# Kernel optimization log

Hardware: AMD Instinct MI355X
Metric: run time of the kernel (lower is better)

Reference implementation:

```python
import jax, jax.numpy as jnp
import numpy as np

B, S, E, H = 2, 2048, 1024, 16
DH = E // H


def setup_inputs() -> dict:
    key = jax.random.key(0)
    ks = jax.random.split(key, 9)
    inp = {
        "query": jax.random.normal(ks[0], (B, S, E), dtype=jnp.float32),
        "key": jax.random.normal(ks[1], (B, S, E), dtype=jnp.float32),
        "value": jax.random.normal(ks[2], (B, S, E), dtype=jnp.float32),
        # causal mask: True means "masked out" (masked_fill semantics)
        "mask": jnp.broadcast_to(
            jnp.triu(jnp.ones((S, S), dtype=bool), k=1)[None, None], (B, 1, S, S)
        ),
        # learned parameters (nn.Linear weight is [out, in]; y = x @ W.T + b)
        "Wq": jax.random.normal(ks[3], (E, E), dtype=jnp.float32) / np.sqrt(E),
        "Wk": jax.random.normal(ks[4], (E, E), dtype=jnp.float32) / np.sqrt(E),
        "Wv": jax.random.normal(ks[5], (E, E), dtype=jnp.float32) / np.sqrt(E),
        "Wo": jax.random.normal(ks[6], (E, E), dtype=jnp.float32) / np.sqrt(E),
        "bo": jax.random.normal(ks[7], (E,), dtype=jnp.float32) * 0.01,
    }
    return inp


def reference(query, key, value, mask, Wq, Wk, Wv, Wo, bo):
    # projections (no bias for q/k/v)
    Q = query @ Wq.T  # [B,S,E]
    K = key @ Wk.T
    V = value @ Wv.T
    # split heads: [B,S,E] -> [B,H,S,Dh]
    Q = Q.reshape(B, S, H, DH).transpose(0, 2, 1, 3)
    K = K.reshape(B, S, H, DH).transpose(0, 2, 1, 3)
    V = V.reshape(B, S, H, DH).transpose(0, 2, 1, 3)
    scale = 1.0 / np.sqrt(DH).astype(np.float32)
    scores = jnp.einsum("bhqd,bhkd->bhqk", Q, K) * scale  # [B,H,S,S]
    scores = jnp.where(mask, -jnp.inf, scores)
    attn = jax.nn.softmax(scores, axis=-1)
    # dropout(p=0.2) is identity in eval mode
    out = jnp.einsum("bhqk,bhkd->bhqd", attn, V)  # [B,H,S,Dh]
    out = out.transpose(0, 2, 1, 3).reshape(B, S, E)
    return out @ Wo.T + bo
```

## Files before the change

### kernel.cpp

```cpp
#include <hip/hip_runtime.h>
#include <hip/hip_bf16.h>
#include <stdint.h>

#define Bb 2
#define Ss 2048
#define Ee 1024
#define Hh 16
#define Dh 64

typedef __bf16 bf16_t;
typedef __attribute__((ext_vector_type(8))) __bf16 bf16x8;
typedef __attribute__((ext_vector_type(4))) __bf16 bf16x4;
typedef __attribute__((ext_vector_type(4))) float f32x4;

#define QSCALE_LOG2E 0.18033688011112042f

__device__ inline void gload_lds16(const void* g, void* l) {
  __builtin_amdgcn_global_load_lds((__attribute__((address_space(1))) void*)g,
                                   (__attribute__((address_space(3))) void*)l,
                                   16, 0, 0);
}

__device__ inline void wg_barrier() {
  asm volatile("s_barrier" ::: "memory");
}

__device__ __forceinline__ int p_addr64(int q, int kv) {
  return q * 128 + ((((kv >> 3) ^ q) & 7) << 4) + (kv & 7) * 2;
}

struct Cvt7 {
  const float* s[7];
  bf16_t* d[7];
  int n8[7];
};

__global__ __launch_bounds__(256) void cvt_f32_bf16(Cvt7 c) {
  int gid = blockIdx.x * 256 + threadIdx.x;
#pragma unroll
  for (int j = 0; j < 7; ++j) {
    if (gid < c.n8[j]) {
      const float* s = c.s[j] + (size_t)gid * 8;
      const f32x4 lo = *(const f32x4*)s;
      const f32x4 hi = *(const f32x4*)(s + 4);
      bf16x8 v;
      v[0] = (bf16_t)lo[0]; v[1] = (bf16_t)lo[1];
      v[2] = (bf16_t)lo[2]; v[3] = (bf16_t)lo[3];
      v[4] = (bf16_t)hi[0]; v[5] = (bf16_t)hi[1];
      v[6] = (bf16_t)hi[2]; v[7] = (bf16_t)hi[3];
      *(bf16x8*)(c.d[j] + (size_t)gid * 8) = v;
      return;
    }
    gid -= c.n8[j];
  }
}

template <int ROWS>
__device__ __forceinline__ void stage_bf16(const bf16_t* __restrict__ src,
                                           int ldk, int k0, bf16_t* lds,
                                           int wave, int lane) {
  const int srow = lane >> 3, sslot = lane & 7;
#pragma unroll
  for (int r = 0; r < ROWS / 32; ++r) {
    const int chunk = wave + r * 4;
    const int row = chunk * 8 + srow;
    const int k16 = sslot ^ (row & 7);
    gload_lds16(src + (size_t)row * ldk + k0 + k16 * 8, lds + chunk * 512);
  }
}

template <typename EPI>
__device__ __forceinline__ void gemm_128x64(const bf16_t* Arow,
                                            const bf16_t* Wrow, bf16_t* As,
                                            bf16_t* Bs, int wave, int lane,
                                            EPI epi) {
  const int lr = lane & 15, lg = lane >> 4;
  f32x4 acc[2][4] = {};

  stage_bf16<128>(Arow, Ee, 0, As, wave, lane);
  stage_bf16<64>(Wrow, Ee, 0, Bs, wave, lane);
  stage_bf16<128>(Arow, Ee, 64, As + 8192, wave, lane);
  stage_bf16<64>(Wrow, Ee, 64, Bs + 4096, wave, lane);

  for (int t = 0; t < 16; ++t) {
    const int cur = t & 1;
    if (t < 15)
      asm volatile("s_waitcnt vmcnt(6)" ::: "memory");
    else
      asm volatile("s_waitcnt vmcnt(0)" ::: "memory");
    wg_barrier();

    const char* a_base = (const char*)(As + cur * 8192);
    const char* b_base = (const char*)(Bs + cur * 4096);
#pragma unroll
    for (int kk = 0; kk < 2; ++kk) {
      bf16x8 af[2], bfr[4];
#pragma unroll
      for (int x = 0; x < 2; ++x) {
        const int arow = wave * 32 + x * 16 + lr;
        af[x] = *(const bf16x8*)(a_base + ((arow * 128 + kk * 64 + lg * 16) ^
                                           ((arow & 7) << 4)));
      }
#pragma unroll
      for (int ni = 0; ni < 4; ++ni) {
        const int brow = ni * 16 + lr;
        bfr[ni] = *(const bf16x8*)(b_base + ((brow * 128 + kk * 64 + lg * 16) ^
                                             ((brow & 7) << 4)));
      }
#pragma unroll
      for (int mi = 0; mi < 2; ++mi)
#pragma unroll
        for (int ni = 0; ni < 4; ++ni)
          acc[mi][ni] = __builtin_amdgcn_mfma_f32_16x16x32_bf16(
              af[mi], bfr[ni], acc[mi][ni], 0, 0, 0);
    }
    wg_barrier();
    if (t + 2 < 16) {
      stage_bf16<128>(Arow, Ee, (t + 2) * 64, As + cur * 8192, wave, lane);
      stage_bf16<64>(Wrow, Ee, (t + 2) * 64, Bs + cur * 4096, wave, lane);
    }
  }

#pragma unroll
  for (int mi = 0; mi < 2; ++mi)
#pragma unroll
    for (int i = 0; i < 4; ++i) {
      const int mloc = wave * 32 + mi * 16 + lg * 4 + i;
#pragma unroll
      for (int ni = 0; ni < 4; ++ni)
        epi(mloc, ni * 16 + lr, acc[mi][ni][i]);
    }
}

__global__ __launch_bounds__(256) void qkv_proj(
    const bf16_t* __restrict__ Aq, const bf16_t* __restrict__ Ak,
    const bf16_t* __restrict__ Av, const bf16_t* __restrict__ Wq,
    const bf16_t* __restrict__ Wk, const bf16_t* __restrict__ Wv,
    bf16_t* __restrict__ Cq, bf16_t* __restrict__ Ck,
    bf16_t* __restrict__ Cv) {
  __shared__ bf16_t As[2][128 * 64];
  __shared__ bf16_t Bs[2][64 * 64];
  const int z = blockIdx.z;
  const bf16_t* A = (z == 0) ? Aq : (z == 1) ? Ak : Av;
  const bf16_t* W = (z == 0) ? Wq : (z == 1) ? Wk : Wv;
  bf16_t* C = (z == 0) ? Cq : (z == 1) ? Ck : Cv;

  const int wg = blockIdx.y * 16 + blockIdx.x;
  const int virt = (wg & 7) * 64 + (wg >> 3);
  const int n0 = (virt & 15) * 64, m0 = (virt >> 4) * 128;

  const int lane = threadIdx.x & 63, wave = threadIdx.x >> 6;

  gemm_128x64(A + (size_t)m0 * Ee, W + (size_t)n0 * Ee, As[0], Bs[0], wave,
              lane, [&](int mloc, int nloc, float v) {
                const int m = m0 + mloc, n = n0 + nloc;
                if (z == 0) v *= QSCALE_LOG2E;
                const int b = m >> 11, s = m & (Ss - 1);
                const int h = n >> 6, d = n & 63;
                if (z != 2)
                  C[(((size_t)(b * Hh + h)) * Ss + s) * Dh + d] = (bf16_t)v;
                else
                  C[(((size_t)(b * Hh + h)) * Dh + d) * Ss + s] = (bf16_t)v;
              });
}

__global__ __launch_bounds__(256) void out_gemm(const bf16_t* __restrict__ A,
                                                const bf16_t* __restrict__ W,
                                                const float* __restrict__ bias,
                                                float* __restrict__ C) {
  __shared__ bf16_t As[2][128 * 64];
  __shared__ bf16_t Bs[2][64 * 64];
  const int wg = blockIdx.y * 16 + blockIdx.x;
  const int virt = (wg & 7) * 64 + (wg >> 3);
  const int n0 = (virt & 15) * 64, m0 = (virt >> 4) * 128;

  const int lane = threadIdx.x & 63, wave = threadIdx.x >> 6;

  gemm_128x64(A + (size_t)m0 * Ee, W + (size_t)n0 * Ee, As[0], Bs[0], wave,
              lane, [&](int mloc, int nloc, float v) {
                const int n = n0 + nloc;
                C[(size_t)(m0 + mloc) * Ee + n] = v + bias[n];
              });
}


__device__ __forceinline__ void attn_stage(const bf16_t* Kh, const bf16_t* Vh,
                                           int kv0, int wave, int lane,
                                           bf16_t* KsBuf, bf16_t* VsBuf) {
#pragma unroll
  for (int r = 0; r < 2; ++r) {
    const int c = wave + r * 4;
    const int row = c * 8 + (lane >> 3);
    const int sl = (lane & 7) ^ (row & 7);
    gload_lds16(Kh + (size_t)(kv0 + row) * Dh + sl * 8, KsBuf + c * 512);
    gload_lds16(Vh + (size_t)row * Ss + kv0 + sl * 8, VsBuf + c * 512);
  }
}

template <bool MASKED>
__device__ __forceinline__ void attn_tile_compute(
    int kv0, int qw, int lane, char* pb, const char* kb, const char* vb,
    const bf16x8 aq[2], float& m_run, float& l_run, f32x4 oacc[4]) {
  const int lr = lane & 15, lg = lane >> 4;

  f32x4 sc[4];
#pragma unroll
  for (int ni = 0; ni < 4; ++ni) {
    const int krow = ni * 16 + lr;
    const bf16x8 ak0 =
        *(const bf16x8*)(kb + ((krow * 128 + lg * 16) ^ ((krow & 7) << 4)));
    const bf16x8 ak1 = *(const bf16x8*)(kb + ((krow * 128 + 64 + lg * 16) ^
                                              ((krow & 7) << 4)));
    f32x4 z = {0.f, 0.f, 0.f, 0.f};
    z = __builtin_amdgcn_mfma_f32_16x16x32_bf16(ak0, aq[0], z, 0, 0, 0);
    z = __builtin_amdgcn_mfma_f32_16x16x32_bf16(ak1, aq[1], z, 0, 0, 0);
    sc[ni] = z;
  }

  if (MASKED) {
    const int q_rel = qw + lr - kv0;
#pragma unroll
    for (int ni = 0; ni < 4; ++ni)
#pragma unroll
      for (int i = 0; i < 4; ++i)
        if (ni * 16 + lg * 4 + i > q_rel) sc[ni][i] = -1e30f;
  }

  f32x4 vm = sc[0];
#pragma unroll
  for (int ni = 1; ni < 4; ++ni)
#pragma unroll
    for (int i = 0; i < 4; ++i) vm[i] = fmaxf(vm[i], sc[ni][i]);
  float rm = fmaxf(fmaxf(vm[0], vm[1]), fmaxf(vm[2], vm[3]));
  rm = fmaxf(rm, __shfl_xor(rm, 16));
  rm = fmaxf(rm, __shfl_xor(rm, 32));

  const float mo = m_run;
  const float mn = fmaxf(mo, rm);
  const float corr = __builtin_amdgcn_exp2f(mo - mn);
  m_run = mn;

  f32x4 vs = {0.f, 0.f, 0.f, 0.f};
#pragma unroll
  for (int ni = 0; ni < 4; ++ni) {
    bf16x4 w;
#pragma unroll
    for (int i = 0; i < 4; ++i) {
      const float p = __builtin_amdgcn_exp2f(sc[ni][i] - mn);
      vs[i] += p;
      w[i] = (bf16_t)p;
    }
    *(bf16x4*)(pb + p_addr64(lr, ni * 16 + lg * 4)) = w;
  }
  float rs = (vs[0] + vs[1]) + (vs[2] + vs[3]);
  rs += __shfl_xor(rs, 16);
  rs += __shfl_xor(rs, 32);
  l_run = l_run * corr + rs;

#pragma unroll
  for (int i = 0; i < 4; ++i) {
    const float ci = __shfl(corr, (lane & 48) | (lg * 4 + i));
#pragma unroll
    for (int di = 0; di < 4; ++di) oacc[di][i] *= ci;
  }

#pragma unroll
  for (int kk = 0; kk < 2; ++kk) {
    const bf16x8 pa = *(const bf16x8*)(pb + p_addr64(lr, kk * 32 + lg * 8));
#pragma unroll
    for (int di = 0; di < 4; ++di) {
      const int vrow = di * 16 + lr;
      const bf16x8 bv = *(const bf16x8*)(vb + ((vrow * 128 + kk * 64 +
                                                lg * 16) ^
                                               ((vrow & 7) << 4)));
      oacc[di] =
          __builtin_amdgcn_mfma_f32_16x16x32_bf16(pa, bv, oacc[di], 0, 0, 0);
    }
  }
}

__global__ __launch_bounds__(256, 4) void attn_causal(
    const bf16_t* __restrict__ Qg, const bf16_t* __restrict__ Kg,
    const bf16_t* __restrict__ Vg, bf16_t* __restrict__ AO) {
  const int wg = blockIdx.y * 32 + blockIdx.x;
  const int virt = (wg & 7) * 128 + (wg >> 3);
  const int bh = virt >> 5;
  const int i_ = virt & 31;
  const int qt = (i_ & 1) ? 31 - (i_ >> 1) : (i_ >> 1);

  const int tid = threadIdx.x;
  const int lane = tid & 63, wave = tid >> 6;
  const int lr = lane & 15, lg = lane >> 4;

  const bf16_t* Qh = Qg + (size_t)bh * Ss * Dh;
  const bf16_t* Kh = Kg + (size_t)bh * Ss * Dh;
  const bf16_t* Vh = Vg + (size_t)bh * Dh * Ss;
  const int b = bh >> 4, h = bh & 15;
  bf16_t* AO_row = AO + (size_t)b * Ss * Ee + h * 64;

  __shared__ bf16_t Ks[2][64 * 64];
  __shared__ bf16_t Vs[2][64 * 64];
  __shared__ bf16_t Ps[4][16 * 64];

  const int qw = qt * 64 + wave * 16;

  bf16x8 aq[2];
#pragma unroll
  for (int kd = 0; kd < 2; ++kd)
    aq[kd] = *(const bf16x8*)(Qh + (size_t)(qw + lr) * Dh + kd * 32 + lg * 8);

  f32x4 oacc[4] = {};
  float m_run = -1e30f, l_run = 0.f;
  char* pb = (char*)Ps[wave];

  const int nt = qt + 1;
  attn_stage(Kh, Vh, 0, wave, lane, Ks[0], Vs[0]);

  for (int t = 0; t < nt; ++t) {
    const int cur = t & 1;
    if (t + 1 < nt) {
      attn_stage(Kh, Vh, (t + 1) * 64, wave, lane, Ks[cur ^ 1], Vs[cur ^ 1]);
      asm volatile("s_waitcnt vmcnt(4)" ::: "memory");
    } else {
      asm volatile("s_waitcnt vmcnt(0)" ::: "memory");
    }
    wg_barrier();
    const char* kb = (const char*)Ks[cur];
    const char* vb = (const char*)Vs[cur];
    if (t < nt - 1)
      attn_tile_compute<false>(t * 64, qw, lane, pb, kb, vb, aq, m_run, l_run,
                               oacc);
    else
      attn_tile_compute<true>(t * 64, qw, lane, pb, kb, vb, aq, m_run, l_run,
                              oacc);
    wg_barrier();
  }

#pragma unroll
  for (int i = 0; i < 4; ++i) {
    const float li = __shfl(l_run, (lane & 48) | (lg * 4 + i));
    const float inv = 1.0f / li;
    const int s = qw + lg * 4 + i;
#pragma unroll
    for (int di = 0; di < 4; ++di) {
      const int d = di * 16 + lr;
      AO_row[(size_t)s * Ee + d] = (bf16_t)(oacc[di][i] * inv);
    }
  }
}

extern "C" void kernel_launch(void* const* d_in, const int* in_sizes, int n_in,
                              void* d_out, int out_size, void* d_ws,
                              size_t ws_size, hipStream_t stream) {
  const float* query = (const float*)d_in[0];
  const float* key = (const float*)d_in[1];
  const float* value = (const float*)d_in[2];
  const float* Wq = (const float*)d_in[4];
  const float* Wk = (const float*)d_in[5];
  const float* Wv = (const float*)d_in[6];
  const float* Wo = (const float*)d_in[7];
  const float* bo = (const float*)d_in[8];

  const size_t T = (size_t)Bb * Ss * Ee;
  const size_t WN = (size_t)Ee * Ee;
  bf16_t* qbf = (bf16_t*)d_ws;
  bf16_t* kbf = qbf + T;
  bf16_t* vbf = kbf + T;
  bf16_t* wqb = vbf + T;
  bf16_t* wkb = wqb + WN;
  bf16_t* wvb = wkb + WN;
  bf16_t* wob = wvb + WN;
  bf16_t* qws = wob + WN;
  bf16_t* kws = qws + T;
  bf16_t* vws = kws + T;
  bf16_t* aows = qbf;

  Cvt7 c;
  c.s[0] = query; c.d[0] = qbf; c.n8[0] = (int)(T / 8);
  c.s[1] = key;   c.d[1] = kbf; c.n8[1] = (int)(T / 8);
  c.s[2] = value; c.d[2] = vbf; c.n8[2] = (int)(T / 8);
  c.s[3] = Wq;    c.d[3] = wqb; c.n8[3] = (int)(WN / 8);
  c.s[4] = Wk;    c.d[4] = wkb; c.n8[4] = (int)(WN / 8);
  c.s[5] = Wv;    c.d[5] = wvb; c.n8[5] = (int)(WN / 8);
  c.s[6] = Wo;    c.d[6] = wob; c.n8[6] = (int)(WN / 8);
  const int total8 = (int)((3 * T + 4 * WN) / 8);

  dim3 blk(256);
  cvt_f32_bf16<<<dim3(total8 / 256), blk, 0, stream>>>(c);
  qkv_proj<<<dim3(Ee / 64, (Bb * Ss) / 128, 3), blk, 0, stream>>>(
      qbf, kbf, vbf, wqb, wkb, wvb, qws, kws, vws);
  attn_causal<<<dim3(32, Bb * Hh), blk, 0, stream>>>(qws, kws, vws, aows);
  out_gemm<<<dim3(Ee / 64, (Bb * Ss) / 128), blk, 0, stream>>>(
      aows, wob, bo, (float*)d_out);
}
```

Measured before the change: 140.1 us.

## Use 128-wide KV tiles and pair causal q-tiles per workgroup

The attention kernel now stages K/V in 128-row tiles with double buffering, which halves the loop iterations and barriers per q-tile. Each workgroup processes two complementary q-tiles (qx and 31-qx), so every block does an equal amount of causal work and the grid is halved. LDS use roughly doubles and occupancy drops to 2 blocks per CU, which may reduce latency hiding. The final diagonal tile is handled with a 64-wide masked variant when the q-tile index is even.

```diff
diff --git a/kernel.cpp b/kernel.cpp
--- a/kernel.cpp
+++ b/kernel.cpp
@@ -25,8 +25,8 @@
   asm volatile("s_barrier" ::: "memory");
 }
 
-__device__ __forceinline__ int p_addr64(int q, int kv) {
-  return q * 128 + ((((kv >> 3) ^ q) & 7) << 4) + (kv & 7) * 2;
+__device__ __forceinline__ int p_addr(int q, int kv) {
+  return q * 256 + ((((kv >> 3) ^ q) & 15) << 4) + (kv & 7) * 2;
 }
 
 struct Cvt7 {
@@ -188,24 +188,26 @@
                                            int kv0, int wave, int lane,
                                            bf16_t* KsBuf, bf16_t* VsBuf) {
 #pragma unroll
-  for (int r = 0; r < 2; ++r) {
+  for (int r = 0; r < 4; ++r) {
     const int c = wave + r * 4;
-    const int row = c * 8 + (lane >> 3);
-    const int sl = (lane & 7) ^ (row & 7);
-    gload_lds16(Kh + (size_t)(kv0 + row) * Dh + sl * 8, KsBuf + c * 512);
-    gload_lds16(Vh + (size_t)row * Ss + kv0 + sl * 8, VsBuf + c * 512);
-  }
-}
-
-template <bool MASKED>
+    const int krow = c * 8 + (lane >> 3);
+    const int ks = (lane & 7) ^ (krow & 7);
+    gload_lds16(Kh + (size_t)(kv0 + krow) * Dh + ks * 8, KsBuf + c * 512);
+    const int vrow = c * 4 + (lane >> 4);
+    const int vs = (lane & 15) ^ (vrow & 7);
+    gload_lds16(Vh + (size_t)vrow * Ss + kv0 + vs * 8, VsBuf + c * 512);
+  }
+}
+
+template <int NI, bool MASKED>
 __device__ __forceinline__ void attn_tile_compute(
     int kv0, int qw, int lane, char* pb, const char* kb, const char* vb,
     const bf16x8 aq[2], float& m_run, float& l_run, f32x4 oacc[4]) {
   const int lr = lane & 15, lg = lane >> 4;
 
-  f32x4 sc[4];
-#pragma unroll
-  for (int ni = 0; ni < 4; ++ni) {
+  f32x4 sc[NI];
+#pragma unroll
+  for (int ni = 0; ni < NI; ++ni) {
     const int krow = ni * 16 + lr;
     const bf16x8 ak0 =
         *(const bf16x8*)(kb + ((krow * 128 + lg * 16) ^ ((krow & 7) << 4)));
@@ -220,7 +222,7 @@
   if (MASKED) {
     const int q_rel = qw + lr - kv0;
 #pragma unroll
-    for (int ni = 0; ni < 4; ++ni)
+    for (int ni = 0; ni < NI; ++ni)
 #pragma unroll
       for (int i = 0; i < 4; ++i)
         if (ni * 16 + lg * 4 + i > q_rel) sc[ni][i] = -1e30f;
@@ -228,7 +230,7 @@
 
   f32x4 vm = sc[0];
 #pragma unroll
-  for (int ni = 1; ni < 4; ++ni)
+  for (int ni = 1; ni < NI; ++ni)
 #pragma unroll
     for (int i = 0; i < 4; ++i) vm[i] = fmaxf(vm[i], sc[ni][i]);
   float rm = fmaxf(fmaxf(vm[0], vm[1]), fmaxf(vm[2], vm[3]));
@@ -242,7 +244,7 @@
 
   f32x4 vs = {0.f, 0.f, 0.f, 0.f};
 #pragma unroll
-  for (int ni = 0; ni < 4; ++ni) {
+  for (int ni = 0; ni < NI; ++ni) {
     bf16x4 w;
 #pragma unroll
     for (int i = 0; i < 4; ++i) {
@@ -250,7 +252,7 @@
       vs[i] += p;
       w[i] = (bf16_t)p;
     }
-    *(bf16x4*)(pb + p_addr64(lr, ni * 16 + lg * 4)) = w;
+    *(bf16x4*)(pb + p_addr(lr, ni * 16 + lg * 4)) = w;
   }
   float rs = (vs[0] + vs[1]) + (vs[2] + vs[3]);
   rs += __shfl_xor(rs, 16);
@@ -265,12 +267,12 @@
   }
 
 #pragma unroll
-  for (int kk = 0; kk < 2; ++kk) {
-    const bf16x8 pa = *(const bf16x8*)(pb + p_addr64(lr, kk * 32 + lg * 8));
+  for (int kk = 0; kk < NI / 2; ++kk) {
+    const bf16x8 pa = *(const bf16x8*)(pb + p_addr(lr, kk * 32 + lg * 8));
 #pragma unroll
     for (int di = 0; di < 4; ++di) {
       const int vrow = di * 16 + lr;
-      const bf16x8 bv = *(const bf16x8*)(vb + ((vrow * 128 + kk * 64 +
+      const bf16x8 bv = *(const bf16x8*)(vb + ((vrow * 256 + kk * 64 +
                                                 lg * 16) ^
                                                ((vrow & 7) << 4)));
       oacc[di] =
@@ -279,18 +281,73 @@
   }
 }
 
-__global__ __launch_bounds__(256, 4) void attn_causal(
+__device__ __forceinline__ void flash_qtile(int qt, const bf16_t* Qh,
+                                            const bf16_t* Kh, const bf16_t* Vh,
+                                            bf16_t* AO_row, int wave, int lane,
+                                            bf16_t* Ks, bf16_t* Vs,
+                                            bf16_t* PsW) {
+  const int lr = lane & 15, lg = lane >> 4;
+  const int qw = qt * 64 + wave * 16;
+
+  bf16x8 aq[2];
+#pragma unroll
+  for (int kd = 0; kd < 2; ++kd)
+    aq[kd] = *(const bf16x8*)(Qh + (size_t)(qw + lr) * Dh + kd * 32 + lg * 8);
+
+  f32x4 oacc[4] = {};
+  float m_run = -1e30f, l_run = 0.f;
+  char* pb = (char*)PsW;
+
+  const int nt = (qt + 2) >> 1;
+  attn_stage(Kh, Vh, 0, wave, lane, Ks, Vs);
+
+  for (int t = 0; t < nt; ++t) {
+    const int cur = t & 1;
+    if (t + 1 < nt) {
+      attn_stage(Kh, Vh, (t + 1) * 128, wave, lane, Ks + (cur ^ 1) * 8192,
+                 Vs + (cur ^ 1) * 8192);
+      asm volatile("s_waitcnt vmcnt(8)" ::: "memory");
+    } else {
+      asm volatile("s_waitcnt vmcnt(0)" ::: "memory");
+    }
+    wg_barrier();
+    const char* kb = (const char*)(Ks + cur * 8192);
+    const char* vb = (const char*)(Vs + cur * 8192);
+    if (t < nt - 1)
+      attn_tile_compute<8, false>(t * 128, qw, lane, pb, kb, vb, aq, m_run,
+                                  l_run, oacc);
+    else if ((qt & 1) == 0)
+      attn_tile_compute<4, true>(t * 128, qw, lane, pb, kb, vb, aq, m_run,
+                                 l_run, oacc);
+    else
+      attn_tile_compute<8, true>(t * 128, qw, lane, pb, kb, vb, aq, m_run,
+                                 l_run, oacc);
+    wg_barrier();
+  }
+
+#pragma unroll
+  for (int i = 0; i < 4; ++i) {
+    const float li = __shfl(l_run, (lane & 48) | (lg * 4 + i));
+    const float inv = 1.0f / li;
+    const int s = qw + lg * 4 + i;
+#pragma unroll
+    for (int di = 0; di < 4; ++di) {
+      const int d = di * 16 + lr;
+      AO_row[(size_t)s * Ee + d] = (bf16_t)(oacc[di][i] * inv);
+    }
+  }
+}
+
+__global__ __launch_bounds__(256, 2) void attn_causal(
     const bf16_t* __restrict__ Qg, const bf16_t* __restrict__ Kg,
     const bf16_t* __restrict__ Vg, bf16_t* __restrict__ AO) {
-  const int wg = blockIdx.y * 32 + blockIdx.x;
-  const int virt = (wg & 7) * 128 + (wg >> 3);
-  const int bh = virt >> 5;
-  const int i_ = virt & 31;
-  const int qt = (i_ & 1) ? 31 - (i_ >> 1) : (i_ >> 1);
+  const int wg = blockIdx.y * 16 + blockIdx.x;
+  const int virt = (wg & 7) * 64 + (wg >> 3);
+  const int qx = virt & 15;
+  const int bh = virt >> 4;
 
   const int tid = threadIdx.x;
   const int lane = tid & 63, wave = tid >> 6;
-  const int lr = lane & 15, lg = lane >> 4;
 
   const bf16_t* Qh = Qg + (size_t)bh * Ss * Dh;
   const bf16_t* Kh = Kg + (size_t)bh * Ss * Dh;
@@ -298,55 +355,14 @@
   const int b = bh >> 4, h = bh & 15;
   bf16_t* AO_row = AO + (size_t)b * Ss * Ee + h * 64;
 
-  __shared__ bf16_t Ks[2][64 * 64];
-  __shared__ bf16_t Vs[2][64 * 64];
-  __shared__ bf16_t Ps[4][16 * 64];
-
-  const int qw = qt * 64 + wave * 16;
-
-  bf16x8 aq[2];
-#pragma unroll
-  for (int kd = 0; kd < 2; ++kd)
-    aq[kd] = *(const bf16x8*)(Qh + (size_t)(qw + lr) * Dh + kd * 32 + lg * 8);
-
-  f32x4 oacc[4] = {};
-  float m_run = -1e30f, l_run = 0.f;
-  char* pb = (char*)Ps[wave];
-
-  const int nt = qt + 1;
-  attn_stage(Kh, Vh, 0, wave, lane, Ks[0], Vs[0]);
-
-  for (int t = 0; t < nt; ++t) {
-    const int cur = t & 1;
-    if (t + 1 < nt) {
-      attn_stage(Kh, Vh, (t + 1) * 64, wave, lane, Ks[cur ^ 1], Vs[cur ^ 1]);
-      asm volatile("s_waitcnt vmcnt(4)" ::: "memory");
-    } else {
-      asm volatile("s_waitcnt vmcnt(0)" ::: "memory");
-    }
-    wg_barrier();
-    const char* kb = (const char*)Ks[cur];
-    const char* vb = (const char*)Vs[cur];
-    if (t < nt - 1)
-      attn_tile_compute<false>(t * 64, qw, lane, pb, kb, vb, aq, m_run, l_run,
-                               oacc);
-    else
-      attn_tile_compute<true>(t * 64, qw, lane, pb, kb, vb, aq, m_run, l_run,
-                              oacc);
-    wg_barrier();
-  }
-
-#pragma unroll
-  for (int i = 0; i < 4; ++i) {
-    const float li = __shfl(l_run, (lane & 48) | (lg * 4 + i));
-    const float inv = 1.0f / li;
-    const int s = qw + lg * 4 + i;
-#pragma unroll
-    for (int di = 0; di < 4; ++di) {
-      const int d = di * 16 + lr;
-      AO_row[(size_t)s * Ee + d] = (bf16_t)(oacc[di][i] * inv);
-    }
-  }
+  __shared__ bf16_t Ks[2][128 * 64];
+  __shared__ bf16_t Vs[2][64 * 128];
+  __shared__ bf16_t Ps[4][16 * 128];
+
+  const int qtA = qx;
+  const int qtB = 31 - qx;
+  flash_qtile(qtA, Qh, Kh, Vh, AO_row, wave, lane, Ks[0], Vs[0], Ps[wave]);
+  flash_qtile(qtB, Qh, Kh, Vh, AO_row, wave, lane, Ks[0], Vs[0], Ps[wave]);
 }
 
 extern "C" void kernel_launch(void* const* d_in, const int* in_sizes, int n_in,
@@ -389,7 +405,7 @@
   cvt_f32_bf16<<<dim3(total8 / 256), blk, 0, stream>>>(c);
   qkv_proj<<<dim3(Ee / 64, (Bb * Ss) / 128, 3), blk, 0, stream>>>(
       qbf, kbf, vbf, wqb, wkb, wvb, qws, kws, vws);
-  attn_causal<<<dim3(32, Bb * Hh), blk, 0, stream>>>(qws, kws, vws, aows);
+  attn_causal<<<dim3(16, Bb * Hh), blk, 0, stream>>>(qws, kws, vws, aows);
   out_gemm<<<dim3(Ee / 64, (Bb * Ss) / 128), blk, 0, stream>>>(
       aows, wob, bo, (float*)d_out);
 }
```

Measured after the change: 113.3 us (median of 3 runs). -19.1%, faster.
